# Performance work log

Measured on AMD Instinct MI355X. Metric: run time of the kernel, lower is better.

## Reference

```python
import jax, jax.numpy as jnp
import numpy as np

C = 128   # d_pair, fixed by the fp8 tri-mul kernel assert
H = 128   # d_hidden


def layer_norm(x, w, b, eps=1e-5):
    m = jnp.mean(x, axis=-1, keepdims=True)
    v = jnp.mean(jnp.square(x - m), axis=-1, keepdims=True)
    return (x - m) * jax.lax.rsqrt(v + eps) * w + b


def setup_inputs() -> dict:
    key = jax.random.key(0)
    ks = jax.random.split(key, 12)
    B, N = 1, 512
    s_in = 1.0 / np.sqrt(C)
    s_h = 1.0 / np.sqrt(H)
    return {
        "z": jax.random.normal(ks[0], (B, N, N, C), jnp.float32),
        "mask": jnp.ones((B, N, N), jnp.float32),
        "ln_in_w": jnp.ones((C,), jnp.float32),
        "ln_in_b": jnp.zeros((C,), jnp.float32),
        "w_ap": jax.random.normal(ks[1], (C, H), jnp.float32) * s_in,
        "b_ap": jnp.zeros((H,), jnp.float32),
        "w_ag": jax.random.normal(ks[2], (C, H), jnp.float32) * s_in,
        "b_ag": jnp.zeros((H,), jnp.float32),
        "w_bp": jax.random.normal(ks[3], (C, H), jnp.float32) * s_in,
        "b_bp": jnp.zeros((H,), jnp.float32),
        "w_bg": jax.random.normal(ks[4], (C, H), jnp.float32) * s_in,
        "b_bg": jnp.zeros((H,), jnp.float32),
        "ln_out_w": jnp.ones((H,), jnp.float32),
        "ln_out_b": jnp.zeros((H,), jnp.float32),
        "w_o": jax.random.normal(ks[5], (H, C), jnp.float32) * s_h,
        "b_o": jnp.zeros((C,), jnp.float32),
        "w_g": jax.random.normal(ks[6], (C, C), jnp.float32) * s_in,
        "b_g": jnp.zeros((C,), jnp.float32),
    }


def reference(z, mask, ln_in_w, ln_in_b, w_ap, b_ap, w_ag, b_ag,
              w_bp, b_bp, w_bg, b_bg, ln_out_w, ln_out_b, w_o, b_o, w_g, b_g):
    # Triangular multiplicative update (outgoing), gated projections.
    z_ln = layer_norm(z, ln_in_w, ln_in_b)                      # [B,N,N,C]
    m = mask[..., None]                                         # [B,N,N,1]
    a = m * jax.nn.sigmoid(z_ln @ w_ag + b_ag) * (z_ln @ w_ap + b_ap)
    b = m * jax.nn.sigmoid(z_ln @ w_bg + b_bg) * (z_ln @ w_bp + b_bp)
    # outgoing: x[b,i,j,c] = sum_k a[b,i,k,c] * b[b,j,k,c]
    x = jnp.einsum("bikc,bjkc->bijc", a, b)                     # [B,N,N,H]
    x = layer_norm(x, ln_out_w, ln_out_b)
    g = jax.nn.sigmoid(z_ln @ w_g + b_g)                        # output gate
    return g * (x @ w_o + b_o)
```

## Files before the change

### kernel.cpp

```cpp
#include <hip/hip_runtime.h>
#include <hip/hip_bf16.h>
#include <stdint.h>

#define NDIM 512
#define NN (NDIM*NDIM)
#define CDIM 128
#define LDSP 136

typedef __attribute__((ext_vector_type(8))) short short8;
typedef __attribute__((ext_vector_type(4))) short short4v;
typedef __attribute__((ext_vector_type(4))) float f32x4;
typedef unsigned long long ull;

__device__ __forceinline__ unsigned short f2bf(float f) {
    union { float f; uint32_t u; } v; v.f = f;
    uint32_t u = v.u;
    return (unsigned short)((u + 0x7FFFu + ((u >> 16) & 1u)) >> 16);
}
__device__ __forceinline__ float bf2f(unsigned short b) {
    union { uint32_t u; float f; } v; v.u = ((uint32_t)b) << 16;
    return v.f;
}
__device__ __forceinline__ f32x4 mfma16(short8 a, short8 b, f32x4 c) {
    return __builtin_amdgcn_mfma_f32_16x16x32_bf16(a, b, c, 0, 0, 0);
}
__device__ __forceinline__ void gl_lds16(const void* g, void* l) {
    __builtin_amdgcn_global_load_lds((const __attribute__((address_space(1))) void*)g,
                                     (__attribute__((address_space(3))) void*)l,
                                     16, 0, 0);
}

__global__ void k0_prep(const float* __restrict__ w_ag, const float* __restrict__ w_ap,
                        const float* __restrict__ w_bg, const float* __restrict__ w_bp,
                        const float* __restrict__ w_g,  const float* __restrict__ w_o,
                        unsigned short* __restrict__ Wfrag, unsigned short* __restrict__ Wo_t)
{
    int idx = blockIdx.x * 256 + threadIdx.x;
    if (idx < 10240) {
        int lane = idx & 63;
        int n  = (idx >> 6) & 3;
        int kk = (idx >> 8) & 3;
        int h  = (idx >> 10) & 1;
        int s  = idx >> 11;
        const float* w = (s==0) ? w_ag : (s==1) ? w_ap : (s==2) ? w_bg : (s==3) ? w_bp : w_g;
        int col = h*64 + n*16 + (lane & 15);
        int k0  = kk*32 + (lane >> 4)*8;
        short8 pk;
        #pragma unroll
        for (int e = 0; e < 8; e++)
            pk[e] = (short)f2bf(w[(k0 + e)*128 + col]);
        *(short8*)(Wfrag + (size_t)idx*8) = pk;
    } else if (idx < 10240 + 16384) {
        int i2 = idx - 10240;
        int cc = i2 >> 7, hh = i2 & 127;
        Wo_t[i2] = f2bf(w_o[hh*128 + cc]);
    }
}

__global__ __launch_bounds__(256, 3) void k1_proj(
    const float* __restrict__ z, const float* __restrict__ mask,
    const float* __restrict__ lnw, const float* __restrict__ lnb,
    const unsigned short* __restrict__ Wfrag,
    const float* __restrict__ b_ag, const float* __restrict__ b_ap,
    const float* __restrict__ b_bg, const float* __restrict__ b_bp,
    const float* __restrict__ b_g,
    unsigned short* __restrict__ a_t, unsigned short* __restrict__ b_t,
    unsigned short* __restrict__ g_out)
{
    __shared__ unsigned short zb[128*LDSP];
    __shared__ float mask_s[128];
    __shared__ float lnw_s[128];
    __shared__ float lnb_s[128];
    __shared__ float bias_s[640];

    const int t = threadIdx.x;
    const int pos0 = blockIdx.x * 128;
    const int tid2 = t >> 1, half = t & 1;
    const int wave = t >> 6, lane = t & 63;
    const int lr = lane & 15, lh = lane >> 4;

    if (t < 128) {
        lnw_s[t] = lnw[t];
        lnb_s[t] = lnb[t];
        mask_s[t] = mask[pos0 + t];
    }
    for (int i = t; i < 640; i += 256) {
        int s = i >> 7, c = i & 127;
        const float* bp = (s==0) ? b_ag : (s==1) ? b_ap : (s==2) ? b_bg : (s==3) ? b_bp : b_g;
        bias_s[i] = bp[c];
    }

    float v[64];
    float s0 = 0.f, s1 = 0.f;
    {
        const float* zr = z + (size_t)(pos0 + tid2) * CDIM + half * 64;
        #pragma unroll
        for (int i = 0; i < 16; i++) {
            float4 q = *(const float4*)(zr + i*4);
            v[i*4+0] = q.x; v[i*4+1] = q.y; v[i*4+2] = q.z; v[i*4+3] = q.w;
        }
        #pragma unroll
        for (int i = 0; i < 64; i++) { s0 += v[i]; s1 += v[i]*v[i]; }
        s0 += __shfl_xor(s0, 1);
        s1 += __shfl_xor(s1, 1);
    }
    __syncthreads();
    {
        float m  = s0 * (1.f/128.f);
        float va = s1 * (1.f/128.f) - m*m;
        float rs = rsqrtf(va + 1e-5f);
        #pragma unroll
        for (int i = 0; i < 8; i++) {
            short8 pk;
            #pragma unroll
            for (int j = 0; j < 8; j++) {
                int c = half*64 + i*8 + j;
                pk[j] = (short)f2bf((v[i*8+j]-m)*rs*lnw_s[c] + lnb_s[c]);
            }
            *(short8*)&zb[tid2*LDSP + half*64 + i*8] = pk;
        }
    }
    __syncthreads();

    const int rowA0 = (wave*32 + lr)*LDSP;
    const int rowA1 = (wave*32 + 16 + lr)*LDSP;
    const unsigned short* wfl = Wfrag + (size_t)lane*8;

    auto gemmh = [&](int s, int h, f32x4 (&acc)[2][4]) {
        #pragma unroll
        for (int m = 0; m < 2; m++)
            #pragma unroll
            for (int n = 0; n < 4; n++) { f32x4 zz = {0.f,0.f,0.f,0.f}; acc[m][n] = zz; }
        const unsigned short* wf = wfl + (size_t)(s*2 + h)*8192;
        #pragma unroll
        for (int kk = 0; kk < 4; kk++) {
            const int k0 = kk*32 + lh*8;
            short8 af0 = *(const short8*)&zb[rowA0 + k0];
            short8 af1 = *(const short8*)&zb[rowA1 + k0];
            #pragma unroll
            for (int n = 0; n < 4; n++) {
                short8 bf = *(const short8*)(wf + (kk*4 + n)*512);
                acc[0][n] = mfma16(af0, bf, acc[0][n]);
                acc[1][n] = mfma16(af1, bf, acc[1][n]);
            }
        }
    };

    auto pair_half = [&](int sG, int sP, int h, unsigned short* dstg) {
        f32x4 G[2][4], P[2][4];
        gemmh(sG, h, G);
        gemmh(sP, h, P);
        const int odd = lh & 1;
        const int base = wave*32 + lh*4 + (odd ? 12 : 0);
        #pragma unroll
        for (int n = 0; n < 4; n++) {
            int col = h*64 + n*16 + lr;
            float bgv = bias_s[sG*128 + col];
            float bpv = bias_s[sP*128 + col];
            union { short4v v; ull u; } p0, p1;
            #pragma unroll
            for (int r = 0; r < 4; r++) {
                float g0 = 1.f / (1.f + __expf(-(G[0][n][r] + bgv)));
                p0.v[r] = (short)f2bf(mask_s[wave*32 + lh*4 + r] * g0 * (P[0][n][r] + bpv));
                float g1 = 1.f / (1.f + __expf(-(G[1][n][r] + bgv)));
                p1.v[r] = (short)f2bf(mask_s[wave*32 + 16 + lh*4 + r] * g1 * (P[1][n][r] + bpv));
            }
            ull r0 = __shfl_xor(p0.u, 16);
            ull r1 = __shfl_xor(p1.u, 16);
            union { ull u[2]; short8 v; } outv;
            outv.u[0] = odd ? r1 : p0.u;
            outv.u[1] = odd ? p1.u : r0;
            *(short8*)(dstg + (size_t)col*NN + pos0 + base) = outv.v;
        }
    };

    pair_half(0, 1, 0, a_t);
    pair_half(0, 1, 1, a_t);
    pair_half(2, 3, 0, b_t);
    pair_half(2, 3, 1, b_t);

    f32x4 G0[2][4], G1[2][4];
    gemmh(4, 0, G0);
    gemmh(4, 1, G1);
    __syncthreads();
    #pragma unroll
    for (int m = 0; m < 2; m++) {
        int rb = wave*32 + m*16 + lh*4;
        #pragma unroll
        for (int n = 0; n < 4; n++) {
            int c0 = n*16 + lr;
            int c1 = 64 + n*16 + lr;
            float b0 = bias_s[512 + c0];
            float b1 = bias_s[512 + c1];
            #pragma unroll
            for (int r = 0; r < 4; r++) {
                zb[(rb + r)*LDSP + c0] = f2bf(1.f / (1.f + __expf(-(G0[m][n][r] + b0))));
                zb[(rb + r)*LDSP + c1] = f2bf(1.f / (1.f + __expf(-(G1[m][n][r] + b1))));
            }
        }
    }
    __syncthreads();
    {
        const unsigned short* src = zb + tid2*LDSP + half*64;
        unsigned short* dst = g_out + (size_t)(pos0 + tid2)*CDIM + half*64;
        #pragma unroll
        for (int i = 0; i < 8; i++)
            *(short8*)(dst + i*8) = *(const short8*)(src + i*8);
    }
}

__global__ __launch_bounds__(256, 2) void k2_einsum(
    const unsigned short* __restrict__ a_t,
    const unsigned short* __restrict__ b_t,
    unsigned short* __restrict__ x_t)
{
    __shared__ unsigned short As[128*64];
    __shared__ unsigned short Bs[128*64];

    const int c  = blockIdx.y;
    const int ti = (blockIdx.x >> 2) * 128;
    const int tj = (blockIdx.x & 3) * 128;
    const int t = threadIdx.x;
    const int wave = t >> 6, lane = t & 63;
    const int lr = lane & 15, lh = lane >> 4;
    const int wm = wave >> 1, wn = wave & 1;

    const unsigned short* Ag = a_t + (size_t)c*NN + (size_t)ti*NDIM;
    const unsigned short* Bg = b_t + (size_t)c*NN + (size_t)tj*NDIM;

    const int srow = wave*32 + (lane >> 3);
    const int scol = (lane & 7) * 8;

    f32x4 acc[4][4] = {};

    for (int k0 = 0; k0 < NDIM; k0 += 64) {
        __syncthreads();
        #pragma unroll
        for (int it = 0; it < 4; it++) {
            int r = srow + it*8;
            gl_lds16(Ag + (size_t)r*NDIM + k0 + scol, (void*)(As + (wave*32 + it*8)*64));
            gl_lds16(Bg + (size_t)r*NDIM + k0 + scol, (void*)(Bs + (wave*32 + it*8)*64));
        }
        asm volatile("s_waitcnt vmcnt(0)" ::: "memory");
        __syncthreads();
        #pragma unroll
        for (int kk = 0; kk < 2; kk++) {
            const int kof = kk*32 + lh*8;
            short8 af[4], bfr[4];
            #pragma unroll
            for (int m = 0; m < 4; m++)
                af[m] = *(const short8*)&As[(wm*64 + m*16 + lr)*64 + kof];
            #pragma unroll
            for (int n = 0; n < 4; n++)
                bfr[n] = *(const short8*)&Bs[(wn*64 + n*16 + lr)*64 + kof];
            #pragma unroll
            for (int m = 0; m < 4; m++)
                #pragma unroll
                for (int n = 0; n < 4; n++)
                    acc[m][n] = mfma16(af[m], bfr[n], acc[m][n]);
        }
    }

    #pragma unroll
    for (int m = 0; m < 4; m++) {
        int row = ti + wm*64 + m*16 + lh*4;
        #pragma unroll
        for (int n = 0; n < 4; n++) {
            int col = tj + wn*64 + n*16 + lr;
            unsigned short* dst = x_t + (size_t)c*NN + (size_t)row*NDIM + col;
            #pragma unroll
            for (int r = 0; r < 4; r++)
                dst[(size_t)r*NDIM] = f2bf(acc[m][n][r]);
        }
    }
}

__global__ __launch_bounds__(256, 2) void k3_out(
    const unsigned short* __restrict__ x_t,
    const unsigned short* __restrict__ g_in,
    const unsigned short* __restrict__ Wo_t,
    const float* __restrict__ lnw, const float* __restrict__ lnb,
    const float* __restrict__ b_o,
    float* __restrict__ out)
{
    __shared__ unsigned short xb[128*LDSP];
    __shared__ unsigned short zl[128*LDSP];
    __shared__ float lnw_s[128];
    __shared__ float lnb_s[128];
    __shared__ float bo_s[128];

    const int t = threadIdx.x;
    const int pos0 = blockIdx.x * 128;
    const int tid2 = t >> 1, half = t & 1;
    const int wave = t >> 6, lane = t & 63;
    const int lr = lane & 15, lh = lane >> 4;

    if (t < 128) { lnw_s[t] = lnw[t]; lnb_s[t] = lnb[t]; bo_s[t] = b_o[t]; }

    {
        const unsigned short* src = x_t + (size_t)tid2*NN + pos0 + half*64;
        unsigned short* dst = xb + tid2*LDSP + half*64;
        #pragma unroll
        for (int i = 0; i < 8; i++)
            *(short8*)(dst + i*8) = *(const short8*)(src + i*8);
    }
    __syncthreads();

    {
        float v[64];
        float s0 = 0.f, s1 = 0.f;
        #pragma unroll
        for (int i = 0; i < 64; i++) {
            float x = bf2f(xb[(half*64 + i)*LDSP + tid2]);
            v[i] = x; s0 += x; s1 += x*x;
        }
        s0 += __shfl_xor(s0, 1);
        s1 += __shfl_xor(s1, 1);
        float m  = s0 * (1.f/128.f);
        float va = s1 * (1.f/128.f) - m*m;
        float rs = rsqrtf(va + 1e-5f);
        #pragma unroll
        for (int i = 0; i < 64; i++) {
            int cc = half*64 + i;
            zl[tid2*LDSP + cc] = f2bf((v[i]-m)*rs*lnw_s[cc] + lnb_s[cc]);
        }
    }
    __syncthreads();

    {
        const unsigned short* src = Wo_t + ((size_t)tid2*128 + half*64);
        unsigned short* dst = xb + tid2*LDSP + half*64;
        #pragma unroll
        for (int i = 0; i < 8; i++)
            *(short8*)(dst + i*8) = *(const short8*)(src + i*8);
    }
    __syncthreads();

    f32x4 acc[2][8];
    #pragma unroll
    for (int m = 0; m < 2; m++)
        #pragma unroll
        for (int n = 0; n < 8; n++) { f32x4 zz = {0.f,0.f,0.f,0.f}; acc[m][n] = zz; }

    #pragma unroll
    for (int kk = 0; kk < 4; kk++) {
        const int k0 = kk*32 + lh*8;
        short8 af0 = *(const short8*)&zl[(wave*32 + lr)*LDSP + k0];
        short8 af1 = *(const short8*)&zl[(wave*32 + 16 + lr)*LDSP + k0];
        #pragma unroll
        for (int n = 0; n < 8; n++) {
            short8 bf = *(const short8*)&xb[(n*16 + lr)*LDSP + k0];
            acc[0][n] = mfma16(af0, bf, acc[0][n]);
            acc[1][n] = mfma16(af1, bf, acc[1][n]);
        }
    }
    __syncthreads();

    {
        const unsigned short* src = g_in + (size_t)(pos0 + tid2)*CDIM + half*64;
        unsigned short* dst = zl + tid2*LDSP + half*64;
        #pragma unroll
        for (int i = 0; i < 8; i++)
            *(short8*)(dst + i*8) = *(const short8*)(src + i*8);
    }
    __syncthreads();

    #pragma unroll
    for (int m = 0; m < 2; m++) {
        int rb = wave*32 + m*16 + lh*4;
        #pragma unroll
        for (int n = 0; n < 8; n++) {
            int col = n*16 + lr;
            float bo = bo_s[col];
            #pragma unroll
            for (int r = 0; r < 4; r++) {
                int row = rb + r;
                float gv = bf2f(zl[row*LDSP + col]);
                out[(size_t)(pos0 + row)*CDIM + col] = gv * (acc[m][n][r] + bo);
            }
        }
    }
}

extern "C" void kernel_launch(void* const* d_in, const int* in_sizes, int n_in,
                              void* d_out, int out_size, void* d_ws, size_t ws_size,
                              hipStream_t stream) {
    const float* z        = (const float*)d_in[0];
    const float* mask     = (const float*)d_in[1];
    const float* ln_in_w  = (const float*)d_in[2];
    const float* ln_in_b  = (const float*)d_in[3];
    const float* w_ap     = (const float*)d_in[4];
    const float* b_ap     = (const float*)d_in[5];
    const float* w_ag     = (const float*)d_in[6];
    const float* b_ag     = (const float*)d_in[7];
    const float* w_bp     = (const float*)d_in[8];
    const float* b_bp     = (const float*)d_in[9];
    const float* w_bg     = (const float*)d_in[10];
    const float* b_bg     = (const float*)d_in[11];
    const float* ln_out_w = (const float*)d_in[12];
    const float* ln_out_b = (const float*)d_in[13];
    const float* w_o      = (const float*)d_in[14];
    const float* b_o      = (const float*)d_in[15];
    const float* w_g      = (const float*)d_in[16];
    const float* b_g      = (const float*)d_in[17];

    char* ws = (char*)d_ws;
    const size_t BUF = (size_t)NN * 128 * 2;
    unsigned short* a_t   = (unsigned short*)(ws);
    unsigned short* b_t   = (unsigned short*)(ws + BUF);
    unsigned short* g_b   = (unsigned short*)(ws + 2*BUF);
    unsigned short* x_t   = (unsigned short*)(ws + 3*BUF);
    unsigned short* Wfrag = (unsigned short*)(ws + 4*BUF);
    unsigned short* Wo_t  = (unsigned short*)(ws + 4*BUF + (size_t)10240*8*2);

    k0_prep<<<104, 256, 0, stream>>>(w_ag, w_ap, w_bg, w_bp, w_g, w_o, Wfrag, Wo_t);
    k1_proj<<<NN/128, 256, 0, stream>>>(z, mask, ln_in_w, ln_in_b, Wfrag,
                                        b_ag, b_ap, b_bg, b_bp, b_g, a_t, b_t, g_b);
    k2_einsum<<<dim3(16, 128), 256, 0, stream>>>(a_t, b_t, x_t);
    k3_out<<<NN/128, 256, 0, stream>>>(x_t, g_b, Wo_t, ln_out_w, ln_out_b, b_o,
                                       (float*)d_out);
}
```

Baseline: 330.9 us.

## Switch intermediates and MFMA from bf16 to fp16, batch weight loads

Replaces the manual bf16 round-to-nearest conversions with native fp16 conversions and uses the f16 MFMA variant throughout all kernels. The projection GEMM now preloads eight weight fragments per stage before issuing MFMAs, and k1's occupancy hint is raised from 3 to 4 blocks. Native half conversion is cheaper than the integer bf16 rounding sequence. The cost is fp16's narrower range: the einsum output over 512 terms could overflow or lose accuracy, and the higher occupancy target may force register spills.

Measured after the change: 348.1 us. 5.2% more time.

```diff
diff --git a/kernel.cpp b/kernel.cpp
--- a/kernel.cpp
+++ b/kernel.cpp
@@ -10,19 +10,22 @@
 typedef __attribute__((ext_vector_type(8))) short short8;
 typedef __attribute__((ext_vector_type(4))) short short4v;
 typedef __attribute__((ext_vector_type(4))) float f32x4;
+typedef __attribute__((ext_vector_type(8))) _Float16 half8;
 typedef unsigned long long ull;
 
-__device__ __forceinline__ unsigned short f2bf(float f) {
-    union { float f; uint32_t u; } v; v.f = f;
-    uint32_t u = v.u;
-    return (unsigned short)((u + 0x7FFFu + ((u >> 16) & 1u)) >> 16);
-}
-__device__ __forceinline__ float bf2f(unsigned short b) {
-    union { uint32_t u; float f; } v; v.u = ((uint32_t)b) << 16;
-    return v.f;
+__device__ __forceinline__ unsigned short f2h(float f) {
+    union { _Float16 h; unsigned short u; } v;
+    v.h = (_Float16)f;
+    return v.u;
+}
+__device__ __forceinline__ float h2f(unsigned short u) {
+    union { _Float16 h; unsigned short u; } v;
+    v.u = u;
+    return (float)v.h;
 }
 __device__ __forceinline__ f32x4 mfma16(short8 a, short8 b, f32x4 c) {
-    return __builtin_amdgcn_mfma_f32_16x16x32_bf16(a, b, c, 0, 0, 0);
+    return __builtin_amdgcn_mfma_f32_16x16x32_f16(
+        __builtin_bit_cast(half8, a), __builtin_bit_cast(half8, b), c, 0, 0, 0);
 }
 __device__ __forceinline__ void gl_lds16(const void* g, void* l) {
     __builtin_amdgcn_global_load_lds((const __attribute__((address_space(1))) void*)g,
@@ -48,16 +51,16 @@
         short8 pk;
         #pragma unroll
         for (int e = 0; e < 8; e++)
-            pk[e] = (short)f2bf(w[(k0 + e)*128 + col]);
+            pk[e] = (short)f2h(w[(k0 + e)*128 + col]);
         *(short8*)(Wfrag + (size_t)idx*8) = pk;
     } else if (idx < 10240 + 16384) {
         int i2 = idx - 10240;
         int cc = i2 >> 7, hh = i2 & 127;
-        Wo_t[i2] = f2bf(w_o[hh*128 + cc]);
-    }
-}
-
-__global__ __launch_bounds__(256, 3) void k1_proj(
+        Wo_t[i2] = f2h(w_o[hh*128 + cc]);
+    }
+}
+
+__global__ __launch_bounds__(256, 4) void k1_proj(
     const float* __restrict__ z, const float* __restrict__ mask,
     const float* __restrict__ lnw, const float* __restrict__ lnb,
     const unsigned short* __restrict__ Wfrag,
@@ -115,7 +118,7 @@
             #pragma unroll
             for (int j = 0; j < 8; j++) {
                 int c = half*64 + i*8 + j;
-                pk[j] = (short)f2bf((v[i*8+j]-m)*rs*lnw_s[c] + lnb_s[c]);
+                pk[j] = (short)f2h((v[i*8+j]-m)*rs*lnw_s[c] + lnb_s[c]);
             }
             *(short8*)&zb[tid2*LDSP + half*64 + i*8] = pk;
         }
@@ -127,21 +130,28 @@
     const unsigned short* wfl = Wfrag + (size_t)lane*8;
 
     auto gemmh = [&](int s, int h, f32x4 (&acc)[2][4]) {
+        const unsigned short* wf = wfl + (size_t)(s*2 + h)*8192;
         #pragma unroll
         for (int m = 0; m < 2; m++)
             #pragma unroll
             for (int n = 0; n < 4; n++) { f32x4 zz = {0.f,0.f,0.f,0.f}; acc[m][n] = zz; }
-        const unsigned short* wf = wfl + (size_t)(s*2 + h)*8192;
-        #pragma unroll
-        for (int kk = 0; kk < 4; kk++) {
-            const int k0 = kk*32 + lh*8;
-            short8 af0 = *(const short8*)&zb[rowA0 + k0];
-            short8 af1 = *(const short8*)&zb[rowA1 + k0];
-            #pragma unroll
-            for (int n = 0; n < 4; n++) {
-                short8 bf = *(const short8*)(wf + (kk*4 + n)*512);
-                acc[0][n] = mfma16(af0, bf, acc[0][n]);
-                acc[1][n] = mfma16(af1, bf, acc[1][n]);
+        #pragma unroll
+        for (int st = 0; st < 2; st++) {
+            short8 wbuf[8];
+            #pragma unroll
+            for (int i = 0; i < 8; i++)
+                wbuf[i] = *(const short8*)(wf + (st*8 + i)*512);
+            #pragma unroll
+            for (int k2 = 0; k2 < 2; k2++) {
+                const int kk = st*2 + k2;
+                const int k0 = kk*32 + lh*8;
+                short8 af0 = *(const short8*)&zb[rowA0 + k0];
+                short8 af1 = *(const short8*)&zb[rowA1 + k0];
+                #pragma unroll
+                for (int n = 0; n < 4; n++) {
+                    acc[0][n] = mfma16(af0, wbuf[k2*4 + n], acc[0][n]);
+                    acc[1][n] = mfma16(af1, wbuf[k2*4 + n], acc[1][n]);
+                }
             }
         }
     };
@@ -161,9 +171,9 @@
             #pragma unroll
             for (int r = 0; r < 4; r++) {
                 float g0 = 1.f / (1.f + __expf(-(G[0][n][r] + bgv)));
-                p0.v[r] = (short)f2bf(mask_s[wave*32 + lh*4 + r] * g0 * (P[0][n][r] + bpv));
+                p0.v[r] = (short)f2h(mask_s[wave*32 + lh*4 + r] * g0 * (P[0][n][r] + bpv));
                 float g1 = 1.f / (1.f + __expf(-(G[1][n][r] + bgv)));
-                p1.v[r] = (short)f2bf(mask_s[wave*32 + 16 + lh*4 + r] * g1 * (P[1][n][r] + bpv));
+                p1.v[r] = (short)f2h(mask_s[wave*32 + 16 + lh*4 + r] * g1 * (P[1][n][r] + bpv));
             }
             ull r0 = __shfl_xor(p0.u, 16);
             ull r1 = __shfl_xor(p1.u, 16);
@@ -194,8 +204,8 @@
             float b1 = bias_s[512 + c1];
             #pragma unroll
             for (int r = 0; r < 4; r++) {
-                zb[(rb + r)*LDSP + c0] = f2bf(1.f / (1.f + __expf(-(G0[m][n][r] + b0))));
-                zb[(rb + r)*LDSP + c1] = f2bf(1.f / (1.f + __expf(-(G1[m][n][r] + b1))));
+                zb[(rb + r)*LDSP + c0] = f2h(1.f / (1.f + __expf(-(G0[m][n][r] + b0))));
+                zb[(rb + r)*LDSP + c1] = f2h(1.f / (1.f + __expf(-(G1[m][n][r] + b1))));
             }
         }
     }
@@ -270,7 +280,7 @@
             unsigned short* dst = x_t + (size_t)c*NN + (size_t)row*NDIM + col;
             #pragma unroll
             for (int r = 0; r < 4; r++)
-                dst[(size_t)r*NDIM] = f2bf(acc[m][n][r]);
+                dst[(size_t)r*NDIM] = f2h(acc[m][n][r]);
         }
     }
 }
@@ -311,7 +321,7 @@
         float s0 = 0.f, s1 = 0.f;
         #pragma unroll
         for (int i = 0; i < 64; i++) {
-            float x = bf2f(xb[(half*64 + i)*LDSP + tid2]);
+            float x = h2f(xb[(half*64 + i)*LDSP + tid2]);
             v[i] = x; s0 += x; s1 += x*x;
         }
         s0 += __shfl_xor(s0, 1);
@@ -322,7 +332,7 @@
         #pragma unroll
         for (int i = 0; i < 64; i++) {
             int cc = half*64 + i;
-            zl[tid2*LDSP + cc] = f2bf((v[i]-m)*rs*lnw_s[cc] + lnb_s[cc]);
+            zl[tid2*LDSP + cc] = f2h((v[i]-m)*rs*lnw_s[cc] + lnb_s[cc]);
         }
     }
     __syncthreads();
@@ -375,7 +385,7 @@
             #pragma unroll
             for (int r = 0; r < 4; r++) {
                 int row = rb + r;
-                float gv = bf2f(zl[row*LDSP + col]);
+                float gv = h2f(zl[row*LDSP + col]);
                 out[(size_t)(pos0 + row)*CDIM + col] = gv * (acc[m][n][r] + bo);
             }
         }
```
